# Kernel optimization log

Hardware: AMD Instinct MI355X
Metric: run time of the kernel (lower is better)

The kernel has to match this reference:

```python
import jax, jax.numpy as jnp
import numpy as np

N = 100000
F_IN = 128
E = 1_600_000
NEG_SLOPE = 0.2  # PyG GATConv default negative_slope


def _seg_sum(v, idx, n):
    return jax.ops.segment_sum(v, idx, num_segments=n)


def gcn_conv(x, W, b, src, dst, n):
    # PyG GCNConv: D^{-1/2} (A + I) D^{-1/2} X W + b (self loops already in src/dst)
    h = x @ W
    deg = _seg_sum(jnp.ones(src.shape, h.dtype), dst, n)
    dinv = jnp.where(deg > 0, jax.lax.rsqrt(deg), 0.0)
    norm = dinv[src] * dinv[dst]  # [E]
    return _seg_sum(h[src] * norm[:, None], dst, n) + b


def gat_conv(x, W, a_src, a_dst, b, src, dst, n, heads, out_ch):
    # PyG GATConv (concat=True), eval mode (dropout inactive)
    h = (x @ W).reshape(n, heads, out_ch)          # [n,H,C]
    s = jnp.einsum('nhc,hc->nh', h, a_src)          # per-node src score
    t = jnp.einsum('nhc,hc->nh', h, a_dst)          # per-node dst score
    e = jax.nn.leaky_relu(s[src] + t[dst], NEG_SLOPE)  # [E,H]
    m = jax.ops.segment_max(e, dst, num_segments=n)    # stable segment softmax
    m = jnp.where(jnp.isfinite(m), m, 0.0)
    p = jnp.exp(e - m[dst])
    denom = _seg_sum(p, dst, n)
    alpha = p / (denom[dst] + 1e-16)                 # [E,H]
    out = _seg_sum(h[src] * alpha[:, :, None], dst, n)  # [n,H,C]
    return out.reshape(n, heads * out_ch) + b


def setup_inputs():
    key = jax.random.key(0)
    ks = jax.random.split(key, 24)
    x = jax.random.normal(ks[0], (N, F_IN), jnp.float32) * 0.1
    half = N // 2
    # one-hot user/item type flags read by forward (x[:,0]==1 / x[:,1]==1)
    x = x.at[:, 0].set(0.0).at[:, 1].set(0.0)
    x = x.at[:half, 0].set(1.0).at[half:, 1].set(1.0)
    src = jax.random.randint(ks[1], (E,), 0, N, dtype=jnp.int32)
    dst = jax.random.randint(ks[2], (E,), 0, N, dtype=jnp.int32)
    edge_index = jnp.stack([src, dst])

    def p(k, shape):
        return jax.random.normal(k, shape, jnp.float32) * 0.1

    inp = {"x": x, "edge_index": edge_index,
           "gcn_w": p(ks[3], (F_IN, 16)), "gcn_b": jnp.zeros((16,), jnp.float32)}
    dims = [(16, 16, 8), (128, 16, 8), (128, 16, 8), (128, 2, 1)]
    for i, (fi, fo, h) in enumerate(dims, start=1):
        inp[f"g{i}_w"] = p(ks[3 + 4 * i], (fi, h * fo))
        inp[f"g{i}_as"] = p(ks[4 + 4 * i], (h, fo))
        inp[f"g{i}_ad"] = p(ks[5 + 4 * i], (h, fo))
        inp[f"g{i}_b"] = jnp.zeros((h * fo,), jnp.float32)
    return inp


def reference(x, edge_index, gcn_w, gcn_b,
              g1_w, g1_as, g1_ad, g1_b,
              g2_w, g2_as, g2_ad, g2_b,
              g3_w, g3_as, g3_ad, g3_b,
              g4_w, g4_as, g4_ad, g4_b):
    n = x.shape[0]
    loops = jnp.arange(n, dtype=edge_index.dtype)  # self loops (added by GCN/GAT layers)
    src = jnp.concatenate([edge_index[0], loops])
    dst = jnp.concatenate([edge_index[1], loops])
    h = jax.nn.elu(gcn_conv(x, gcn_w, gcn_b, src, dst, n))
    h = jax.nn.elu(gat_conv(h, g1_w, g1_as, g1_ad, g1_b, src, dst, n, 8, 16))
    h = jax.nn.elu(gat_conv(h, g2_w, g2_as, g2_ad, g2_b, src, dst, n, 8, 16))
    h = jax.nn.elu(gat_conv(h, g3_w, g3_as, g3_ad, g3_b, src, dst, n, 8, 16))
    h = jax.nn.elu(gat_conv(h, g4_w, g4_as, g4_ad, g4_b, src, dst, n, 1, 2))  # [n,2]
    half = n // 2  # users are rows [:half], items rows [half:]
    out = jnp.concatenate([h[:half], h[half:]], axis=1)  # [half,4]
    return jax.nn.log_softmax(out, axis=1)
```

## Files before the change

kernel.cpp:

```cpp
#include <hip/hip_runtime.h>
#include <cstddef>
#include <cstdint>

#define NN 100000
#define NPAD 100032
#define NE 1600000
#define ET (NE + NN)
#define ETP_MAX (ET + 8 * NN)
#define HALFN (NN / 2)
#define NEG_SLOPE 0.2f
#define SCB 1024
#define RP 8
#define RNODES (NN / RP)
#define CHUNK 8192

typedef __attribute__((ext_vector_type(8))) short short8v;
typedef __attribute__((ext_vector_type(4))) float float4v;
typedef __attribute__((ext_vector_type(2))) float float2v;

__device__ __forceinline__ float lrelu(float x) { return x > 0.f ? x : NEG_SLOPE * x; }

__device__ __forceinline__ uint16_t f2bf(float f) {
  uint32_t u = __float_as_uint(f);
  uint32_t r = u + 0x7fffu + ((u >> 16) & 1u);
  return (uint16_t)(r >> 16);
}
__device__ __forceinline__ float bflo(uint32_t u) { return __uint_as_float(u << 16); }
__device__ __forceinline__ float bfhi(uint32_t u) { return __uint_as_float(u & 0xffff0000u); }

template<int K, int M>
__launch_bounds__(256)
__global__ void gemm4_kernel(const float* __restrict__ X, const float* __restrict__ W,
                             float* __restrict__ Y, int n) {
  constexpr int CG = M / 4;
  constexpr int RG = 256 / CG;
  constexpr int RPT = 2;
  constexpr int RT = RG * RPT;
  constexpr int KP = K + 1;
  __shared__ __align__(16) float sW[K * M];
  __shared__ float sX[RT * KP];
  for (int i = threadIdx.x; i < K * M; i += 256) sW[i] = W[i];
  const int jg = threadIdx.x % CG;
  const int rg = threadIdx.x / CG;
  const int r0 = rg * RPT;
  for (int base = blockIdx.x * RT; base < n; base += gridDim.x * RT) {
    __syncthreads();
    const int nrows = (n - base) < RT ? (n - base) : RT;
    for (int i = threadIdx.x; i < nrows * K; i += 256) {
      int r = i / K, c = i - r * K;
      sX[r * KP + c] = X[(size_t)base * K + i];
    }
    __syncthreads();
    float acc[RPT][4];
    #pragma unroll
    for (int rr = 0; rr < RPT; ++rr) acc[rr][0] = acc[rr][1] = acc[rr][2] = acc[rr][3] = 0.f;
    #pragma unroll 4
    for (int k = 0; k < K; ++k) {
      const float4 w = *(const float4*)&sW[k * M + jg * 4];
      #pragma unroll
      for (int rr = 0; rr < RPT; ++rr) {
        const float xv = sX[(r0 + rr) * KP + k];
        acc[rr][0] = fmaf(xv, w.x, acc[rr][0]);
        acc[rr][1] = fmaf(xv, w.y, acc[rr][1]);
        acc[rr][2] = fmaf(xv, w.z, acc[rr][2]);
        acc[rr][3] = fmaf(xv, w.w, acc[rr][3]);
      }
    }
    #pragma unroll
    for (int rr = 0; rr < RPT; ++rr) {
      if (r0 + rr < nrows) {
        float4 o = make_float4(acc[rr][0], acc[rr][1], acc[rr][2], acc[rr][3]);
        *(float4*)&Y[(size_t)(base + r0 + rr) * M + jg * 4] = o;
      }
    }
  }
}

template<int KB>
__launch_bounds__(256)
__global__ void wpack_kernel(const float* __restrict__ W, uint16_t* __restrict__ wp,
                             int Kreal) {
  int tid = blockIdx.x * 256 + threadIdx.x;
  if (tid >= KB * 8 * 64) return;
  int lane = tid & 63;
  int ctkb = tid >> 6;
  int kb = ctkb % KB, ct = ctkb / KB;
  int nc = ct * 16 + (lane & 15);
  int k0 = kb * 32 + (lane >> 4) * 8;
  ushort4 o0, o1;
  uint16_t v[8];
  #pragma unroll
  for (int j = 0; j < 8; ++j) {
    int k = k0 + j;
    v[j] = (k < Kreal) ? f2bf(W[(size_t)k * 128 + nc]) : (uint16_t)0;
  }
  o0.x = v[0]; o0.y = v[1]; o0.z = v[2]; o0.w = v[3];
  o1.x = v[4]; o1.y = v[5]; o1.z = v[6]; o1.w = v[7];
  *(ushort4*)&wp[(size_t)tid * 8] = o0;
  *(ushort4*)&wp[(size_t)tid * 8 + 4] = o1;
}

template<int KB, int XS>
__launch_bounds__(256)
__global__ void gemm_mfma_kernel(const uint16_t* __restrict__ X,
                                 const uint16_t* __restrict__ wp,
                                 const float* __restrict__ aS, const float* __restrict__ aD,
                                 uint16_t* __restrict__ Y,
                                 float* __restrict__ S, float* __restrict__ T, int n) {
  __shared__ float sC[4][16 * 136];
  const int wv = threadIdx.x >> 6;
  const int lane = threadIdx.x & 63;
  const int rowbase = blockIdx.x * 64 + wv * 16;
  int arow = rowbase + (lane & 15);
  if (arow >= n) arow = n - 1;
  const uint16_t* xp = X + (size_t)arow * XS + ((lane >> 4) * 8);
  short8v a[KB];
  #pragma unroll
  for (int kb = 0; kb < KB; ++kb) a[kb] = *(const short8v*)(xp + kb * 32);
  #pragma unroll
  for (int ct = 0; ct < 8; ++ct) {
    float4v acc = {0.f, 0.f, 0.f, 0.f};
    #pragma unroll
    for (int kb = 0; kb < KB; ++kb) {
      short8v b = *(const short8v*)&wp[(size_t)((ct * KB + kb) * 64 + lane) * 8];
      acc = __builtin_amdgcn_mfma_f32_16x16x32_bf16(a[kb], b, acc, 0, 0, 0);
    }
    #pragma unroll
    for (int r = 0; r < 4; ++r)
      sC[wv][((lane >> 4) * 4 + r) * 136 + ct * 16 + (lane & 15)] = acc[r];
  }
  #pragma unroll
  for (int t = 0; t < 4; ++t) {
    int idx = t * 64 + lane;
    int row = idx >> 4;
    int c8 = idx & 15;
    const float* pr = &sC[wv][row * 136 + c8 * 8];
    float4 lo = *(const float4*)pr;
    float4 hi = *(const float4*)(pr + 4);
    uint4 o;
    o.x = (uint32_t)f2bf(lo.x) | ((uint32_t)f2bf(lo.y) << 16);
    o.y = (uint32_t)f2bf(lo.z) | ((uint32_t)f2bf(lo.w) << 16);
    o.z = (uint32_t)f2bf(hi.x) | ((uint32_t)f2bf(hi.y) << 16);
    o.w = (uint32_t)f2bf(hi.z) | ((uint32_t)f2bf(hi.w) << 16);
    *(uint4*)&Y[(size_t)(rowbase + row) * 128 + c8 * 8] = o;
  }
  {
    int r = lane & 15;
    int hg = lane >> 4;
    int node = rowbase + r;
    if (node < n) {
      #pragma unroll
      for (int hh = 0; hh < 2; ++hh) {
        int h = hg * 2 + hh;
        float sv = 0.f, tv = 0.f;
        #pragma unroll
        for (int c = 0; c < 16; ++c) {
          float v = sC[wv][r * 136 + h * 16 + c];
          sv = fmaf(v, aS[h * 16 + c], sv);
          tv = fmaf(v, aD[h * 16 + c], tv);
        }
        S[(size_t)node * 8 + h] = sv;
        T[(size_t)node * 8 + h] = tv;
      }
    }
  }
}

template<int K, int ROWS>
__launch_bounds__(256)
__global__ void gemm_s2_kernel(const uint16_t* __restrict__ Xb, const float* __restrict__ W,
                               const float* __restrict__ aS, const float* __restrict__ aD,
                               float* __restrict__ Y, float* __restrict__ S,
                               float* __restrict__ T, int n) {
  constexpr int KP = K + 1;
  __shared__ float sW[K * 2];
  __shared__ float sX[ROWS * KP];
  if (blockIdx.x == 0 && threadIdx.x == 0) {
    S[NN] = -1e30f; T[NN] = 0.f;
    Y[(size_t)NN * 2] = 0.f; Y[(size_t)NN * 2 + 1] = 0.f;
  }
  for (int i = threadIdx.x; i < K * 2; i += 256) sW[i] = W[i];
  const float as0 = aS[0], as1 = aS[1], ad0 = aD[0], ad1 = aD[1];
  for (int base = blockIdx.x * ROWS; base < n; base += gridDim.x * ROWS) {
    __syncthreads();
    const int nrows = (n - base) < ROWS ? (n - base) : ROWS;
    for (int i = threadIdx.x; i < nrows * (K / 4); i += 256) {
      int r = i / (K / 4), c = i - r * (K / 4);
      uint2 u = *(const uint2*)&Xb[(size_t)(base + r) * K + c * 4];
      sX[r * KP + c * 4 + 0] = bflo(u.x);
      sX[r * KP + c * 4 + 1] = bfhi(u.x);
      sX[r * KP + c * 4 + 2] = bflo(u.y);
      sX[r * KP + c * 4 + 3] = bfhi(u.y);
    }
    __syncthreads();
    for (int r = threadIdx.x; r < nrows; r += 256) {
      float a0 = 0.f, a1 = 0.f;
      #pragma unroll 4
      for (int k = 0; k < K; ++k) {
        float xv = sX[r * KP + k];
        a0 = fmaf(xv, sW[k * 2], a0);
        a1 = fmaf(xv, sW[k * 2 + 1], a1);
      }
      int node = base + r;
      float2 o; o.x = a0; o.y = a1;
      *(float2*)&Y[(size_t)node * 2] = o;
      S[node] = a0 * as0 + a1 * as1;
      T[node] = a0 * ad0 + a1 * ad1;
    }
  }
}

__launch_bounds__(256)
__global__ void deg_int_kernel(const int* __restrict__ edst, int* __restrict__ degi) {
  int e = blockIdx.x * 256 + threadIdx.x;
  if (e >= ET) return;
  int dn = e < NE ? edst[e] : e - NE;
  atomicAdd(&degi[dn], 1);
}

__device__ __forceinline__ int pad4i(int d) { return (d + 3) & ~3; }

__launch_bounds__(256)
__global__ void scan1_kernel(const int* __restrict__ degi, int* __restrict__ rowptr,
                             int* __restrict__ bsums) {
  __shared__ int sd[256];
  int t = threadIdx.x;
  int base = blockIdx.x * SCB + t * 4;
  int v0 = base + 0 < NN ? pad4i(degi[base + 0]) : 0;
  int v1 = base + 1 < NN ? pad4i(degi[base + 1]) : 0;
  int v2 = base + 2 < NN ? pad4i(degi[base + 2]) : 0;
  int v3 = base + 3 < NN ? pad4i(degi[base + 3]) : 0;
  int s = v0 + v1 + v2 + v3;
  sd[t] = s;
  __syncthreads();
  for (int off = 1; off < 256; off <<= 1) {
    int x = (t >= off) ? sd[t - off] : 0;
    __syncthreads();
    sd[t] += x;
    __syncthreads();
  }
  int excl = sd[t] - s;
  if (t == 255) bsums[blockIdx.x] = sd[255];
  if (base + 0 < NN) rowptr[base + 0] = excl;
  excl += v0;
  if (base + 1 < NN) rowptr[base + 1] = excl;
  excl += v1;
  if (base + 2 < NN) rowptr[base + 2] = excl;
  excl += v2;
  if (base + 3 < NN) rowptr[base + 3] = excl;
}

__launch_bounds__(256)
__global__ void scan2_kernel(int* __restrict__ bsums, int nb) {
  __shared__ int sd[256];
  int t = threadIdx.x;
  int v = t < nb ? bsums[t] : 0;
  sd[t] = v;
  __syncthreads();
  for (int off = 1; off < 256; off <<= 1) {
    int x = (t >= off) ? sd[t - off] : 0;
    __syncthreads();
    sd[t] += x;
    __syncthreads();
  }
  if (t < nb) bsums[t] = sd[t] - v;
  if (t == nb - 1) bsums[nb] = sd[t];
}

__launch_bounds__(256)
__global__ void scan3_kernel(int* __restrict__ rowptr, const int* __restrict__ bsums, int nb,
                             const int* __restrict__ deg, float* __restrict__ dinv,
                             float* __restrict__ S8, float* __restrict__ T8,
                             int* __restrict__ csr) {
  int i = blockIdx.x * 256 + threadIdx.x;
  if (i == 0) {
    rowptr[NN] = bsums[nb];
    dinv[NN] = 0.f;
    #pragma unroll
    for (int h = 0; h < 8; ++h) {
      S8[(size_t)NN * 8 + h] = -1e30f;
      T8[(size_t)NN * 8 + h] = 0.f;
    }
  }
  if (i >= NN) return;
  int rp = rowptr[i] + bsums[i / SCB];
  rowptr[i] = rp;
  int dg = deg[i];
  dinv[i] = dg > 0 ? rsqrtf((float)dg) : 0.f;
  int pe = rp + pad4i(dg);
  for (int e = rp + dg; e < pe; ++e) csr[e] = NN;
}

__launch_bounds__(256)
__global__ void scatter_part_kernel(const int* __restrict__ esrc, const int* __restrict__ edst,
                                    const int* __restrict__ rowptr, int* __restrict__ cur2,
                                    int* __restrict__ csr_src) {
  int p = blockIdx.x & (RP - 1);
  int c = blockIdx.x >> 3;
  int lo = p * RNODES, hi = lo + RNODES;
  int e0 = c * CHUNK;
  int e1 = e0 + CHUNK < ET ? e0 + CHUNK : ET;
  for (int e = e0 + threadIdx.x; e < e1; e += 256) {
    int dn = e < NE ? edst[e] : e - NE;
    if (dn >= lo && dn < hi) {
      int sn = e < NE ? esrc[e] : e - NE;
      int slot = rowptr[dn] + atomicAdd(&cur2[dn], 1);
      csr_src[slot] = sn;
    }
  }
}

__launch_bounds__(256)
__global__ void fused_gat_kernel(const int* __restrict__ rowptr, const int* __restrict__ csr,
                                 const float* __restrict__ S, const float* __restrict__ T,
                                 const uint16_t* __restrict__ Hm, const float* __restrict__ bias,
                                 uint16_t* __restrict__ Outb) {
  const int lane = threadIdx.x & 63;
  const int d = (blockIdx.x * 256 + threadIdx.x) >> 6;
  if (d >= NN) return;
  const int rs = rowptr[d];
  const int deg = rowptr[d + 1] - rs;
  const int deg8 = deg & ~7;
  const int eg = lane >> 4;
  const int cl = lane & 15;
  const int hp = cl >> 1;
  const float Th = T[(size_t)d * 8 + hp];
  const char* sb = (const char*)S;
  const char* hb = (const char*)Hm;
  float m = -1e38f;
  float s = 0.f;
  float2v A0 = {0.f, 0.f}, A1 = {0.f, 0.f}, A2 = {0.f, 0.f}, A3 = {0.f, 0.f};
  const uint32_t clo = (uint32_t)(cl << 4);
  const uint32_t hpo = (uint32_t)(hp << 2);
  int iA = rs + eg;
  int snA = csr[iA];
  int snB = csr[iA + 4];
  for (int l0 = 0; l0 < deg8; l0 += 8) {
    int snA2 = csr[iA + 8];
    int snB2 = csr[iA + 12];
    uint4 uA = *(const uint4*)(hb + (((uint32_t)snA << 8) + clo));
    uint4 uB = *(const uint4*)(hb + (((uint32_t)snB << 8) + clo));
    float svA = *(const float*)(sb + (((uint32_t)snA << 5) + hpo));
    float svB = *(const float*)(sb + (((uint32_t)snB << 5) + hpo));
    iA += 8;
    float eA = lrelu(svA + Th);
    float eB = lrelu(svB + Th);
    float nm = fmaxf(m, fmaxf(eA, eB));
    if (nm > m) {
      float sc = __expf(m - nm);
      float2v scv = {sc, sc};
      s *= sc;
      A0 *= scv; A1 *= scv; A2 *= scv; A3 *= scv;
      m = nm;
    }
    float pA = __expf(eA - m);
    float pB = __expf(eB - m);
    s += pA + pB;
    float2v ppA = {pA, pA}, ppB = {pB, pB};
    A0 = ppA * (float2v){bflo(uA.x), bfhi(uA.x)} + A0;
    A1 = ppA * (float2v){bflo(uA.y), bfhi(uA.y)} + A1;
    A2 = ppA * (float2v){bflo(uA.z), bfhi(uA.z)} + A2;
    A3 = ppA * (float2v){bflo(uA.w), bfhi(uA.w)} + A3;
    A0 = ppB * (float2v){bflo(uB.x), bfhi(uB.x)} + A0;
    A1 = ppB * (float2v){bflo(uB.y), bfhi(uB.y)} + A1;
    A2 = ppB * (float2v){bflo(uB.z), bfhi(uB.z)} + A2;
    A3 = ppB * (float2v){bflo(uB.w), bfhi(uB.w)} + A3;
    snA = snA2; snB = snB2;
  }
  if (deg & 4) {
    uint4 uA = *(const uint4*)(hb + (((uint32_t)snA << 8) + clo));
    float svA = *(const float*)(sb + (((uint32_t)snA << 5) + hpo));
    float eA = lrelu(svA + Th);
    float nm = fmaxf(m, eA);
    if (nm > m) {
      float sc = __expf(m - nm);
      float2v scv = {sc, sc};
      s *= sc;
      A0 *= scv; A1 *= scv; A2 *= scv; A3 *= scv;
      m = nm;
    }
    float pA = __expf(eA - m);
    s += pA;
    float2v ppA = {pA, pA};
    A0 = ppA * (float2v){bflo(uA.x), bfhi(uA.x)} + A0;
    A1 = ppA * (float2v){bflo(uA.y), bfhi(uA.y)} + A1;
    A2 = ppA * (float2v){bflo(uA.z), bfhi(uA.z)} + A2;
    A3 = ppA * (float2v){bflo(uA.w), bfhi(uA.w)} + A3;
  }
  #pragma unroll
  for (int mask = 16; mask <= 32; mask <<= 1) {
    float om = __shfl_xor(m, mask);
    float os = __shfl_xor(s, mask);
    float o0x = __shfl_xor(A0.x, mask), o0y = __shfl_xor(A0.y, mask);
    float o1x = __shfl_xor(A1.x, mask), o1y = __shfl_xor(A1.y, mask);
    float o2x = __shfl_xor(A2.x, mask), o2y = __shfl_xor(A2.y, mask);
    float o3x = __shfl_xor(A3.x, mask), o3y = __shfl_xor(A3.y, mask);
    float nm = fmaxf(m, om);
    float s1 = __expf(m - nm), s2 = __expf(om - nm);
    s = s * s1 + os * s2;
    A0.x = A0.x * s1 + o0x * s2; A0.y = A0.y * s1 + o0y * s2;
    A1.x = A1.x * s1 + o1x * s2; A1.y = A1.y * s1 + o1y * s2;
    A2.x = A2.x * s1 + o2x * s2; A2.y = A2.y * s1 + o2y * s2;
    A3.x = A3.x * s1 + o3x * s2; A3.y = A3.y * s1 + o3y * s2;
    m = nm;
  }
  {
    float2v Blo = (eg & 1) ? A1 : A0;
    float2v Bhi = (eg & 1) ? A3 : A2;
    float2v B = (eg & 2) ? Bhi : Blo;
    const float inv = 1.f / (s + 1e-16f);
    float2 b = *(const float2*)&bias[cl * 8 + eg * 2];
    float v0 = fmaf(B.x, inv, b.x);
    float v1 = fmaf(B.y, inv, b.y);
    v0 = v0 > 0.f ? v0 : expm1f(v0);
    v1 = v1 > 0.f ? v1 : expm1f(v1);
    uint32_t o = (uint32_t)f2bf(v0) | ((uint32_t)f2bf(v1) << 16);
    *(uint32_t*)&Outb[(size_t)d * 128 + cl * 8 + eg * 2] = o;
  }
}

__launch_bounds__(256)
__global__ void fused_gat1_kernel(const int* __restrict__ rowptr, const int* __restrict__ csr,
                                  const float* __restrict__ S, const float* __restrict__ T,
                                  const float* __restrict__ Hm2, const float* __restrict__ bias,
                                  float* __restrict__ Out) {
  int lane = threadIdx.x & 63;
  int sub = lane >> 4, l16 = lane & 15;
  int d = ((blockIdx.x * 256 + threadIdx.x) >> 6) * 4 + sub;
  if (d >= NN) return;
  int rs = rowptr[d], deg = rowptr[d + 1] - rs;
  float Td = T[d];
  float m = -1e38f, sAcc = 0.f, a0 = 0.f, a1 = 0.f;
  for (int l = l16; l < deg; l += 16) {
    int sn = csr[rs + l];
    float2 hv = *(const float2*)&Hm2[(size_t)sn * 2];
    float sv = S[sn];
    float e = lrelu(sv + Td);
    float nm = fmaxf(m, e);
    if (e > m) {
      float sc = __expf(m - nm);
      sAcc *= sc; a0 *= sc; a1 *= sc; m = nm;
    }
    float p = __expf(e - m);
    sAcc += p;
    a0 = fmaf(p, hv.x, a0);
    a1 = fmaf(p, hv.y, a1);
  }
  #pragma unroll
  for (int mask = 1; mask <= 8; mask <<= 1) {
    float om = __shfl_xor(m, mask);
    float os = __shfl_xor(sAcc, mask);
    float oa0 = __shfl_xor(a0, mask);
    float oa1 = __shfl_xor(a1, mask);
    float nm = fmaxf(m, om);
    float s1 = __expf(m - nm), s2 = __expf(om - nm);
    sAcc = sAcc * s1 + os * s2;
    a0 = a0 * s1 + oa0 * s2;
    a1 = a1 * s1 + oa1 * s2;
    m = nm;
  }
  if (l16 == 0) {
    float inv = 1.f / (sAcc + 1e-16f);
    float v0 = fmaf(a0, inv, bias[0]);
    float v1 = fmaf(a1, inv, bias[1]);
    v0 = v0 > 0.f ? v0 : expm1f(v0);
    v1 = v1 > 0.f ? v1 : expm1f(v1);
    float2 o; o.x = v0; o.y = v1;
    *(float2*)&Out[(size_t)d * 2] = o;
  }
}

__launch_bounds__(256)
__global__ void gcn_pull_kernel(const int* __restrict__ rowptr, const int* __restrict__ csr_src,
                                const float* __restrict__ dinv, const float* __restrict__ Hm,
                                const float* __restrict__ bias, uint16_t* __restrict__ Outb) {
  int lane = threadIdx.x & 63;
  int d = (blockIdx.x * 256 + threadIdx.x) >> 6;
  if (d >= NN) return;
  int eg = lane >> 4, f = lane & 15;
  int rs = rowptr[d], deg = rowptr[d + 1] - rs;
  float acc = 0.f;
  for (int l = eg; l < deg; l += 4) {
    int sn = csr_src[l + rs];
    acc = fmaf(dinv[sn], Hm[(size_t)sn * 16 + f], acc);
  }
  acc += __shfl_xor(acc, 16);
  acc += __shfl_xor(acc, 32);
  if (eg == 0) {
    float v = acc * dinv[d] + bias[f];
    v = v > 0.f ? v : expm1f(v);
    Outb[(size_t)d * 32 + f] = f2bf(v);
    Outb[(size_t)d * 32 + 16 + f] = 0;
  }
}

__launch_bounds__(256)
__global__ void final_kernel(const float* __restrict__ A, float* __restrict__ Out) {
  int i = blockIdx.x * 256 + threadIdx.x;
  if (i >= HALFN) return;
  float v0 = A[(size_t)i * 2 + 0];
  float v1 = A[(size_t)i * 2 + 1];
  float v2 = A[(size_t)(i + HALFN) * 2 + 0];
  float v3 = A[(size_t)(i + HALFN) * 2 + 1];
  float m = fmaxf(fmaxf(v0, v1), fmaxf(v2, v3));
  float e0 = __expf(v0 - m), e1 = __expf(v1 - m), e2 = __expf(v2 - m), e3 = __expf(v3 - m);
  float l = logf(e0 + e1 + e2 + e3) + m;
  Out[(size_t)i * 4 + 0] = v0 - l;
  Out[(size_t)i * 4 + 1] = v1 - l;
  Out[(size_t)i * 4 + 2] = v2 - l;
  Out[(size_t)i * 4 + 3] = v3 - l;
}

extern "C" void kernel_launch(void* const* d_in, const int* in_sizes, int n_in,
                              void* d_out, int out_size, void* d_ws, size_t ws_size,
                              hipStream_t stream) {
  const float* x     = (const float*)d_in[0];
  const int*   eidx  = (const int*)d_in[1];
  const int*   esrc  = eidx;
  const int*   edst  = eidx + NE;
  const float* gcn_w = (const float*)d_in[2];
  const float* gcn_b = (const float*)d_in[3];

  char* ws = (char*)d_ws;
  uint16_t* hbf    = (uint16_t*)(ws + 0);
  uint16_t* bufAb  = (uint16_t*)(ws + 25700000);
  uint16_t* gcnHbf = (uint16_t*)(ws + 51400000);
  float*    bufB   = (float*)   (ws + 57900000);
  float*    bufC   = (float*)   (ws + 64400000);
  float*    Sb     = (float*)   (ws + 65300000);
  float*    Tb     = (float*)   (ws + 68600000);
  int*      rowptr = (int*)     (ws + 151900000);
  int*      cursor = (int*)     (ws + 152300008);
  int*      csr    = (int*)     (ws + 152700008);
  float*    dinv   = (float*)   (ws + 162700008);
  int*      bsums  = (int*)     (ws + 163100016);
  int*      cur2   = (int*)     (ws + 163100528);
  uint16_t* wpck   = (uint16_t*)(ws + 169900528);

  constexpr int NB_SCAN = (NN + SCB - 1) / SCB;

  hipMemsetAsync(cursor, 0, (size_t)NN * 4, stream);
  hipMemsetAsync(cur2, 0, (size_t)NN * 4, stream);
  deg_int_kernel<<<(ET + 255) / 256, 256, 0, stream>>>(edst, cursor);
  scan1_kernel<<<NB_SCAN, 256, 0, stream>>>(cursor, rowptr, bsums);
  scan2_kernel<<<1, 256, 0, stream>>>(bsums, NB_SCAN);
  scan3_kernel<<<(NN + 256) / 256, 256, 0, stream>>>(rowptr, bsums, NB_SCAN,
                                                     cursor, dinv, Sb, Tb, csr);
  {
    int nch = (ET + CHUNK - 1) / CHUNK;
    scatter_part_kernel<<<nch * RP, 256, 0, stream>>>(esrc, edst, rowptr, cur2, csr);
  }

  {
    int tiles = (NN + 127) / 128;
    if (tiles > 4096) tiles = 4096;
    gemm4_kernel<128, 16><<<tiles, 256, 0, stream>>>(x, gcn_w, bufB, NN);
  }
  gcn_pull_kernel<<<(NN * 64 + 255) / 256, 256, 0, stream>>>(
      rowptr, csr, dinv, bufB, gcn_b, gcnHbf);

  wpack_kernel<1><<<2, 256, 0, stream>>>((const float*)d_in[4], wpck, 16);
  gemm_mfma_kernel<1, 32><<<NPAD / 64, 256, 0, stream>>>(
      gcnHbf, wpck, (const float*)d_in[5], (const float*)d_in[6], hbf, Sb, Tb, NN);
  fused_gat_kernel<<<(NN * 64 + 255) / 256, 256, 0, stream>>>(
      rowptr, csr, Sb, Tb, hbf, (const float*)d_in[7], bufAb);

  wpack_kernel<4><<<8, 256, 0, stream>>>((const float*)d_in[8], wpck, 128);
  gemm_mfma_kernel<4, 128><<<NPAD / 64, 256, 0, stream>>>(
      bufAb, wpck, (const float*)d_in[9], (const float*)d_in[10], hbf, Sb, Tb, NN);
  fused_gat_kernel<<<(NN * 64 + 255) / 256, 256, 0, stream>>>(
      rowptr, csr, Sb, Tb, hbf, (const float*)d_in[11], bufAb);

  wpack_kernel<4><<<8, 256, 0, stream>>>((const float*)d_in[12], wpck, 128);
  gemm_mfma_kernel<4, 128><<<NPAD / 64, 256, 0, stream>>>(
      bufAb, wpck, (const float*)d_in[13], (const float*)d_in[14], hbf, Sb, Tb, NN);
  fused_gat_kernel<<<(NN * 64 + 255) / 256, 256, 0, stream>>>(
      rowptr, csr, Sb, Tb, hbf, (const float*)d_in[15], bufAb);

  {
    int tiles = (NN + 127) / 128;
    if (tiles > 2048) tiles = 2048;
    gemm_s2_kernel<128, 128><<<tiles, 256, 0, stream>>>(
        bufAb, (const float*)d_in[16], (const float*)d_in[17], (const float*)d_in[18],
        bufB, Sb, Tb, NN);
    fused_gat1_kernel<<<(NN * 16 + 255) / 256, 256, 0, stream>>>(
        rowptr, csr, Sb, Tb, bufB, (const float*)d_in[19], bufC);
  }

  final_kernel<<<(HALFN + 255) / 256, 256, 0, stream>>>(bufC, (float*)d_out);
}
```

Baseline: 573.3 us.

## Record atomic ranks at degree count, merge weight packing, narrow GCN pull

The degree-count kernel now saves each edge's atomic slot index, so the CSR scatter writes directly to rowptr+rank. This drops the second atomic pass and the second memset, at the cost of an extra edge-sized int array write and read. The three weight-pack launches become one kernel writing to separate buffers, which removes two launches. The GCN pull now uses 16 lanes per node with a 4-way unrolled loop instead of 64 lanes plus shuffles, which cuts idle lanes but serializes each node's edges within one thread.

```diff
diff --git a/kernel.cpp b/kernel.cpp
--- a/kernel.cpp
+++ b/kernel.cpp
@@ -76,28 +76,31 @@
   }
 }
 
-template<int KB>
-__launch_bounds__(256)
-__global__ void wpack_kernel(const float* __restrict__ W, uint16_t* __restrict__ wp,
-                             int Kreal) {
+__launch_bounds__(256)
+__global__ void wpack_all_kernel(const float* __restrict__ W0, const float* __restrict__ W1,
+                                 const float* __restrict__ W2, uint16_t* __restrict__ wp) {
   int tid = blockIdx.x * 256 + threadIdx.x;
-  if (tid >= KB * 8 * 64) return;
-  int lane = tid & 63;
-  int ctkb = tid >> 6;
+  const float* W; int Kreal, KB, base, t;
+  if (tid < 512)       { W = W0; Kreal = 16;  KB = 1; base = 0;     t = tid; }
+  else if (tid < 2560) { W = W1; Kreal = 128; KB = 4; base = 4096;  t = tid - 512; }
+  else if (tid < 4608) { W = W2; Kreal = 128; KB = 4; base = 20480; t = tid - 2560; }
+  else return;
+  int lane = t & 63;
+  int ctkb = t >> 6;
   int kb = ctkb % KB, ct = ctkb / KB;
   int nc = ct * 16 + (lane & 15);
   int k0 = kb * 32 + (lane >> 4) * 8;
-  ushort4 o0, o1;
   uint16_t v[8];
   #pragma unroll
   for (int j = 0; j < 8; ++j) {
     int k = k0 + j;
     v[j] = (k < Kreal) ? f2bf(W[(size_t)k * 128 + nc]) : (uint16_t)0;
   }
+  ushort4 o0, o1;
   o0.x = v[0]; o0.y = v[1]; o0.z = v[2]; o0.w = v[3];
   o1.x = v[4]; o1.y = v[5]; o1.z = v[6]; o1.w = v[7];
-  *(ushort4*)&wp[(size_t)tid * 8] = o0;
-  *(ushort4*)&wp[(size_t)tid * 8 + 4] = o1;
+  *(ushort4*)&wp[(size_t)base + (size_t)t * 8] = o0;
+  *(ushort4*)&wp[(size_t)base + (size_t)t * 8 + 4] = o1;
 }
 
 template<int KB, int XS>
@@ -211,11 +214,12 @@
 }
 
 __launch_bounds__(256)
-__global__ void deg_int_kernel(const int* __restrict__ edst, int* __restrict__ degi) {
+__global__ void rank_kernel(const int* __restrict__ edst, int* __restrict__ cursor,
+                            int* __restrict__ rank) {
   int e = blockIdx.x * 256 + threadIdx.x;
   if (e >= ET) return;
   int dn = e < NE ? edst[e] : e - NE;
-  atomicAdd(&degi[dn], 1);
+  rank[e] = atomicAdd(&cursor[dn], 1);
 }
 
 __device__ __forceinline__ int pad4i(int d) { return (d + 3) & ~3; }
@@ -293,7 +297,7 @@
 
 __launch_bounds__(256)
 __global__ void scatter_part_kernel(const int* __restrict__ esrc, const int* __restrict__ edst,
-                                    const int* __restrict__ rowptr, int* __restrict__ cur2,
+                                    const int* __restrict__ rowptr, const int* __restrict__ rank,
                                     int* __restrict__ csr_src) {
   int p = blockIdx.x & (RP - 1);
   int c = blockIdx.x >> 3;
@@ -304,8 +308,7 @@
     int dn = e < NE ? edst[e] : e - NE;
     if (dn >= lo && dn < hi) {
       int sn = e < NE ? esrc[e] : e - NE;
-      int slot = rowptr[dn] + atomicAdd(&cur2[dn], 1);
-      csr_src[slot] = sn;
+      csr_src[rowptr[dn] + rank[e]] = sn;
     }
   }
 }
@@ -474,24 +477,28 @@
 __global__ void gcn_pull_kernel(const int* __restrict__ rowptr, const int* __restrict__ csr_src,
                                 const float* __restrict__ dinv, const float* __restrict__ Hm,
                                 const float* __restrict__ bias, uint16_t* __restrict__ Outb) {
-  int lane = threadIdx.x & 63;
-  int d = (blockIdx.x * 256 + threadIdx.x) >> 6;
+  int d = blockIdx.x * 16 + threadIdx.x / 16;
   if (d >= NN) return;
-  int eg = lane >> 4, f = lane & 15;
-  int rs = rowptr[d], deg = rowptr[d + 1] - rs;
+  int f = threadIdx.x & 15;
+  int rs = rowptr[d], re = rowptr[d + 1];
   float acc = 0.f;
-  for (int l = eg; l < deg; l += 4) {
-    int sn = csr_src[l + rs];
+  int j = rs;
+  for (; j + 4 <= re; j += 4) {
+    int s0 = csr_src[j], s1 = csr_src[j + 1], s2 = csr_src[j + 2], s3 = csr_src[j + 3];
+    float d0 = dinv[s0], d1 = dinv[s1], d2 = dinv[s2], d3 = dinv[s3];
+    float h0 = Hm[(size_t)s0 * 16 + f], h1 = Hm[(size_t)s1 * 16 + f];
+    float h2 = Hm[(size_t)s2 * 16 + f], h3 = Hm[(size_t)s3 * 16 + f];
+    acc = fmaf(d0, h0, acc); acc = fmaf(d1, h1, acc);
+    acc = fmaf(d2, h2, acc); acc = fmaf(d3, h3, acc);
+  }
+  for (; j < re; ++j) {
+    int sn = csr_src[j];
     acc = fmaf(dinv[sn], Hm[(size_t)sn * 16 + f], acc);
   }
-  acc += __shfl_xor(acc, 16);
-  acc += __shfl_xor(acc, 32);
-  if (eg == 0) {
-    float v = acc * dinv[d] + bias[f];
-    v = v > 0.f ? v : expm1f(v);
-    Outb[(size_t)d * 32 + f] = f2bf(v);
-    Outb[(size_t)d * 32 + 16 + f] = 0;
-  }
+  float v = acc * dinv[d] + bias[f];
+  v = v > 0.f ? v : expm1f(v);
+  Outb[(size_t)d * 32 + f] = f2bf(v);
+  Outb[(size_t)d * 32 + 16 + f] = 0;
 }
 
 __launch_bounds__(256)
@@ -529,51 +536,51 @@
   float*    bufC   = (float*)   (ws + 64400000);
   float*    Sb     = (float*)   (ws + 65300000);
   float*    Tb     = (float*)   (ws + 68600000);
+  uint16_t* wpck   = (uint16_t*)(ws + 71900000);
   int*      rowptr = (int*)     (ws + 151900000);
   int*      cursor = (int*)     (ws + 152300008);
   int*      csr    = (int*)     (ws + 152700008);
   float*    dinv   = (float*)   (ws + 162700008);
   int*      bsums  = (int*)     (ws + 163100016);
-  int*      cur2   = (int*)     (ws + 163100528);
-  uint16_t* wpck   = (uint16_t*)(ws + 169900528);
+  int*      rank   = (int*)     (ws + 163100528);
+  uint16_t* w0p    = wpck;
+  uint16_t* w1p    = wpck + 4096;
+  uint16_t* w2p    = wpck + 20480;
 
   constexpr int NB_SCAN = (NN + SCB - 1) / SCB;
 
   hipMemsetAsync(cursor, 0, (size_t)NN * 4, stream);
-  hipMemsetAsync(cur2, 0, (size_t)NN * 4, stream);
-  deg_int_kernel<<<(ET + 255) / 256, 256, 0, stream>>>(edst, cursor);
+  rank_kernel<<<(ET + 255) / 256, 256, 0, stream>>>(edst, cursor, rank);
   scan1_kernel<<<NB_SCAN, 256, 0, stream>>>(cursor, rowptr, bsums);
   scan2_kernel<<<1, 256, 0, stream>>>(bsums, NB_SCAN);
   scan3_kernel<<<(NN + 256) / 256, 256, 0, stream>>>(rowptr, bsums, NB_SCAN,
                                                      cursor, dinv, Sb, Tb, csr);
   {
     int nch = (ET + CHUNK - 1) / CHUNK;
-    scatter_part_kernel<<<nch * RP, 256, 0, stream>>>(esrc, edst, rowptr, cur2, csr);
-  }
+    scatter_part_kernel<<<nch * RP, 256, 0, stream>>>(esrc, edst, rowptr, rank, csr);
+  }
+  wpack_all_kernel<<<18, 256, 0, stream>>>((const float*)d_in[4], (const float*)d_in[8],
+                                           (const float*)d_in[12], wpck);
 
   {
     int tiles = (NN + 127) / 128;
     if (tiles > 4096) tiles = 4096;
     gemm4_kernel<128, 16><<<tiles, 256, 0, stream>>>(x, gcn_w, bufB, NN);
   }
-  gcn_pull_kernel<<<(NN * 64 + 255) / 256, 256, 0, stream>>>(
-      rowptr, csr, dinv, bufB, gcn_b, gcnHbf);
-
-  wpack_kernel<1><<<2, 256, 0, stream>>>((const float*)d_in[4], wpck, 16);
+  gcn_pull_kernel<<<(NN + 15) / 16, 256, 0, stream>>>(rowptr, csr, dinv, bufB, gcn_b, gcnHbf);
+
   gemm_mfma_kernel<1, 32><<<NPAD / 64, 256, 0, stream>>>(
-      gcnHbf, wpck, (const float*)d_in[5], (const float*)d_in[6], hbf, Sb, Tb, NN);
+      gcnHbf, w0p, (const float*)d_in[5], (const float*)d_in[6], hbf, Sb, Tb, NN);
   fused_gat_kernel<<<(NN * 64 + 255) / 256, 256, 0, stream>>>(
       rowptr, csr, Sb, Tb, hbf, (const float*)d_in[7], bufAb);
 
-  wpack_kernel<4><<<8, 256, 0, stream>>>((const float*)d_in[8], wpck, 128);
   gemm_mfma_kernel<4, 128><<<NPAD / 64, 256, 0, stream>>>(
-      bufAb, wpck, (const float*)d_in[9], (const float*)d_in[10], hbf, Sb, Tb, NN);
+      bufAb, w1p, (const float*)d_in[9], (const float*)d_in[10], hbf, Sb, Tb, NN);
   fused_gat_kernel<<<(NN * 64 + 255) / 256, 256, 0, stream>>>(
       rowptr, csr, Sb, Tb, hbf, (const float*)d_in[11], bufAb);
 
-  wpack_kernel<4><<<8, 256, 0, stream>>>((const float*)d_in[12], wpck, 128);
   gemm_mfma_kernel<4, 128><<<NPAD / 64, 256, 0, stream>>>(
-      bufAb, wpck, (const float*)d_in[13], (const float*)d_in[14], hbf, Sb, Tb, NN);
+      bufAb, w2p, (const float*)d_in[13], (const float*)d_in[14], hbf, Sb, Tb, NN);
   fused_gat_kernel<<<(NN * 64 + 255) / 256, 256, 0, stream>>>(
       rowptr, csr, Sb, Tb, hbf, (const float*)d_in[15], bufAb);
 
```

Measured after the change: 503.2 us. 12.2% less time.
